# Kernel optimization log

Hardware: AMD Instinct MI355X
Metric: run time of the kernel (lower is better)

Reference implementation:

```python
import jax, jax.numpy as jnp
import numpy as np

W_DIM = 512
FREQ = 1024
CH = 512
OUT_CH = 512
SIZE = 64
SR = 64.0
BW = 2.0
MAX_BW = BW * 8.0
B = 16
K = 3


def setup_inputs() -> dict:
    key = jax.random.key(0)
    ks = jax.random.split(key, 10)
    w = jax.random.normal(ks[0], (B, W_DIM), dtype=jnp.float32)
    # SynthesisInput buffers: random unit-direction freqs scaled by uniform radius in [0, max_bw)
    f = jax.random.normal(ks[1], (FREQ, 2), dtype=jnp.float32)
    f = f / jnp.linalg.norm(f, axis=1, keepdims=True)
    freqs = f * (jax.random.uniform(ks[2], (FREQ, 1), dtype=jnp.float32) * MAX_BW)
    phases = jax.random.uniform(ks[3], (FREQ,), dtype=jnp.float32) - 0.5
    input_weight = jax.random.normal(ks[4], (CH, FREQ), dtype=jnp.float32)
    # affine: FullyConnectedLayer(w_dim, 4, weight_init=0, bias_init=[1,0,0,0])
    affine_w = jnp.zeros((4, W_DIM), dtype=jnp.float32)
    affine_b = jnp.array([1.0, 0.0, 0.0, 0.0], dtype=jnp.float32)
    # per-layer style affine (w -> in_channels), bias_init=1 (StyleGAN convention)
    style_w = jax.random.normal(ks[5], (CH, W_DIM), dtype=jnp.float32)
    style_b = jnp.ones((CH,), dtype=jnp.float32)
    conv_w = jax.random.normal(ks[6], (OUT_CH, CH, K, K), dtype=jnp.float32)
    conv_b = jnp.zeros((OUT_CH,), dtype=jnp.float32)
    return {"w": w, "affine_w": affine_w, "affine_b": affine_b, "freqs": freqs,
            "phases": phases, "input_weight": input_weight, "style_w": style_w,
            "style_b": style_b, "conv_w": conv_w, "conv_b": conv_b}


def _fc(x, weight, bias):
    # FullyConnectedLayer: weight_gain = 1/sqrt(in_features)
    gain = 1.0 / np.sqrt(weight.shape[1])
    return x @ (weight * gain).T + bias


def _synthesis_input(w, affine_w, affine_b, freqs, phases, input_weight):
    t = _fc(w, affine_w, affine_b)                                  # [B,4]
    t = t / jnp.linalg.norm(t[:, :2], axis=1, keepdims=True)
    c, s, tx, ty = t[:, 0], t[:, 1], t[:, 2], t[:, 3]
    # m = m_r @ m_t (only the 2x3 top block matters)
    rot = jnp.stack([jnp.stack([c, -s], -1), jnp.stack([s, c], -1)], 1)  # [B,2,2]
    trans = jnp.stack([-tx, -ty], -1)                               # [B,2]
    shift = jnp.einsum('bij,bj->bi', rot, trans)                    # [B,2]
    phases_b = phases[None, :] + jnp.einsum('fi,bi->bf', freqs, shift)
    freqs_b = jnp.einsum('fi,bij->bfj', freqs, rot)                 # [B,F,2]
    amp = jnp.clip(1.0 - (jnp.linalg.norm(freqs_b, axis=2) - BW) / (SR / 2.0 - BW), 0.0, 1.0)
    # affine_grid(theta=diag(0.5*size/sr)=0.5, align_corners=False)
    theta00 = 0.5 * SIZE / SR
    xs = ((jnp.arange(SIZE, dtype=jnp.float32) + 0.5) / SIZE * 2.0 - 1.0) * theta00
    ys = ((jnp.arange(SIZE, dtype=jnp.float32) + 0.5) / SIZE * 2.0 - 1.0) * theta00
    gx, gy = jnp.meshgrid(xs, ys)                                   # [H,W]
    grid = jnp.stack([gx, gy], axis=-1)                             # [H,W,2]
    x = jnp.einsum('hwi,bfi->bhwf', grid, freqs_b) + phases_b[:, None, None, :]
    x = jnp.sin(x * (2.0 * np.pi)) * amp[:, None, None, :]
    effect_freq = jnp.sum((jnp.linalg.norm(freqs, axis=-1) < BW).astype(jnp.float32))
    x = jnp.einsum('bhwf,cf->bchw', x, input_weight / jnp.sqrt(effect_freq))
    return x                                                        # [B,CH,H,W]


def _modulated_conv2d(x, weight, s, padding=1):
    # demodulate: pre-normalize w and s
    w_hat = weight * jax.lax.rsqrt(jnp.mean(jnp.square(weight), axis=(1, 2, 3), keepdims=True))
    s_hat = s * jax.lax.rsqrt(jnp.mean(jnp.square(s)))
    # dcoefs[b,o] = rsqrt(sum_ikl (w[o,i,k,l]*s[b,i])^2 + eps)
    dcoefs = jax.lax.rsqrt(jnp.einsum('oikl,bi->bo', jnp.square(w_hat), jnp.square(s_hat)) + 1e-8)
    # grouped-per-sample conv == scale input channels by s, conv with base w, scale out by dcoefs
    x = x * s_hat[:, :, None, None]
    y = jax.lax.conv_general_dilated(x, w_hat, window_strides=(1, 1),
                                     padding=[(padding, padding), (padding, padding)],
                                     dimension_numbers=('NCHW', 'OIHW', 'NCHW'))
    return y * dcoefs[:, :, None, None]


def reference(w, affine_w, affine_b, freqs, phases, input_weight, style_w, style_b, conv_w, conv_b):
    x = _synthesis_input(w, affine_w, affine_b, freqs, phases, input_weight)
    s = _fc(w, style_w, style_b)                                    # [B,CH]
    y = _modulated_conv2d(x, conv_w, s, padding=K // 2)
    y = y + conv_b[None, :, None, None]
    y = jnp.where(y >= 0, y, 0.2 * y) * np.sqrt(2.0)                # lrelu + gain (bias_act)
    y = jnp.clip(y, -256.0, 256.0)                                  # conv_clamp
    return y
```

## Files before the change

kernel.cpp:

```cpp
#include <hip/hip_runtime.h>

typedef __attribute__((ext_vector_type(4))) float f32x4;
typedef __attribute__((ext_vector_type(8))) __bf16 bf16x8;

__device__ __forceinline__ unsigned short f2bf(float f) {
  unsigned int u = __builtin_bit_cast(unsigned int, f);
  return (unsigned short)((u + 0x7FFFu + ((u >> 16) & 1u)) >> 16);
}

__device__ __forceinline__ float sin2pi(float x) {
#if __has_builtin(__builtin_amdgcn_sinf) && __has_builtin(__builtin_amdgcn_fractf)
  return __builtin_amdgcn_sinf(__builtin_amdgcn_fractf(x));
#else
  return __sinf(x * 6.283185307179586f);
#endif
}

__device__ __forceinline__ void gll16(const void* g, void* l) {
  __builtin_amdgcn_global_load_lds(
      (const __attribute__((address_space(1))) void*)g,
      (__attribute__((address_space(3))) void*)l, 16, 0, 0);
}

template <int W>
__device__ __forceinline__ void vmwait() {
  if constexpr (W == 0) asm volatile("s_waitcnt vmcnt(0)" ::: "memory");
  else if constexpr (W == 2) asm volatile("s_waitcnt vmcnt(2)" ::: "memory");
  else if constexpr (W == 4) asm volatile("s_waitcnt vmcnt(4)" ::: "memory");
  else if constexpr (W == 6) asm volatile("s_waitcnt vmcnt(6)" ::: "memory");
  else if constexpr (W == 8) asm volatile("s_waitcnt vmcnt(8)" ::: "memory");
}

#define CFENCE() asm volatile("" ::: "memory")

__global__ void prep_freq_k(const float* __restrict__ w, const float* __restrict__ affine_w,
                            const float* __restrict__ affine_b, const float* __restrict__ freqs,
                            const float* __restrict__ phases, float4* __restrict__ freq_data,
                            float* __restrict__ scal) {
  const int b = blockIdx.x, tid = threadIdx.x;
  const int wv = tid >> 6, lane = tid & 63;
  __shared__ float tdot[4];
  __shared__ float par[4];
  __shared__ float scnt;
  float sum = 0.f;
  for (int i = lane; i < 512; i += 64) sum += w[b * 512 + i] * affine_w[wv * 512 + i];
#pragma unroll
  for (int o = 32; o > 0; o >>= 1) sum += __shfl_down(sum, o);
  if (lane == 0) tdot[wv] = sum;
  if (tid == 0) scnt = 0.f;
  __syncthreads();
  if (tid == 0) {
    const float gain = 0.04419417382415922f;
    float t0 = tdot[0] * gain + affine_b[0];
    float t1 = tdot[1] * gain + affine_b[1];
    float t2 = tdot[2] * gain + affine_b[2];
    float t3 = tdot[3] * gain + affine_b[3];
    float inv = 1.f / sqrtf(t0 * t0 + t1 * t1);
    float c = t0 * inv, s = t1 * inv, tx = t2 * inv, ty = t3 * inv;
    par[0] = c; par[1] = s;
    par[2] = -c * tx + s * ty;
    par[3] = -s * tx - c * ty;
  }
  __syncthreads();
  const float c = par[0], s = par[1], sh0 = par[2], sh1 = par[3];
  float cnt = 0.f;
  for (int f = tid; f < 1024; f += 256) {
    float fx = freqs[2 * f], fy = freqs[2 * f + 1];
    float fb0 = fx * c + fy * s;
    float fb1 = fy * c - fx * s;
    float ph = phases[f] + fx * sh0 + fy * sh1;
    float nb = sqrtf(fb0 * fb0 + fb1 * fb1);
    float amp = fminf(fmaxf(1.f - (nb - 2.f) * (1.f / 30.f), 0.f), 1.f);
    float4 v; v.x = fb0; v.y = fb1; v.z = ph; v.w = amp;
    freq_data[(b << 10) + f] = v;
    if (sqrtf(fx * fx + fy * fy) < 2.f) cnt += 1.f;
  }
  if (b == 0) {
    atomicAdd(&scnt, cnt);
    __syncthreads();
    if (tid == 0) scal[0] = 1.f / sqrtf(scnt);
  }
}

__global__ void style_k(const float* __restrict__ w, const float* __restrict__ style_w,
                        const float* __restrict__ style_b, float* __restrict__ s_out) {
  int gt = blockIdx.x * 256 + threadIdx.x;
  int idx = gt >> 2, part = gt & 3;
  int b = idx >> 9, c = idx & 511;
  const float4* wr = (const float4*)(w + b * 512) + part * 32;
  const float4* sr = (const float4*)(style_w + (size_t)c * 512) + part * 32;
  float sum = 0.f;
#pragma unroll 4
  for (int i = 0; i < 32; ++i) {
    float4 a = wr[i], q = sr[i];
    sum += a.x * q.x + a.y * q.y + a.z * q.z + a.w * q.w;
  }
  sum += __shfl_xor(sum, 1);
  sum += __shfl_xor(sum, 2);
  if (part == 0) s_out[idx] = sum * 0.04419417382415922f + style_b[c];
}

__global__ void convw_prep_k(const float* __restrict__ conv_w, float* __restrict__ wsumT,
                             unsigned short* __restrict__ bt_conv) {
  const int o = blockIdx.x, tid = threadIdx.x;
  __shared__ float red[256];
  float sum = 0.f;
  for (int i = tid; i < 4608; i += 256) { float v = conv_w[o * 4608 + i]; sum += v * v; }
  red[tid] = sum;
  __syncthreads();
  for (int off = 128; off > 0; off >>= 1) {
    if (tid < off) red[tid] += red[tid + off];
    __syncthreads();
  }
  const float rn = rsqrtf(red[0] * (1.f / 4608.f));
  for (int i = tid; i < 512; i += 256) {
    float sq = 0.f;
#pragma unroll
    for (int kl = 0; kl < 9; ++kl) {
      float v = conv_w[(o * 512 + i) * 9 + kl];
      sq += v * v;
      bt_conv[o * 4608 + kl * 512 + i] = f2bf(v * rn);
    }
    wsumT[i * 512 + o] = sq * rn * rn;
  }
}

__global__ void iw_cast_k(const float* __restrict__ iw, unsigned short* __restrict__ iw_bf) {
  int i = blockIdx.x * 256 + threadIdx.x;
  iw_bf[i] = f2bf(iw[i]);
}

__global__ void shat_dcoef_k(const float* __restrict__ s, const float* __restrict__ wsumT,
                             float* __restrict__ s_hat, float* __restrict__ dcoefs) {
  const int b = blockIdx.x >> 3, og = blockIdx.x & 7, tid = threadIdx.x;
  __shared__ float red[256];
  __shared__ float sh2[512];
  __shared__ float red2[256];
  float sum = 0.f;
  for (int i = tid; i < 8192; i += 256) { float v = s[i]; sum += v * v; }
  red[tid] = sum;
  __syncthreads();
  for (int off = 128; off > 0; off >>= 1) {
    if (tid < off) red[tid] += red[tid + off];
    __syncthreads();
  }
  const float inv_rms = rsqrtf(red[0] * (1.f / 8192.f));
  for (int c = tid; c < 512; c += 256) {
    float sh = s[b * 512 + c] * inv_rms;
    if (og == 0) s_hat[b * 512 + c] = sh;
    sh2[c] = sh * sh;
  }
  __syncthreads();
  const int o = (og << 6) + (tid & 63);
  const int ic = tid >> 6;
  float acc = 0.f;
  for (int i = ic * 128; i < ic * 128 + 128; ++i) acc += wsumT[i * 512 + o] * sh2[i];
  red2[tid] = acc;
  __syncthreads();
  if (tid < 64) {
    float a = red2[tid] + red2[tid + 64] + red2[tid + 128] + red2[tid + 192];
    dcoefs[b * 512 + o] = rsqrtf(a + 1e-8f);
  }
}

__global__ void border_zero_k(unsigned short* __restrict__ xmp) {
  int idx = blockIdx.x * 256 + threadIdx.x;
  int chunk = idx & 63;
  int t = idx >> 6;
  int p = t % 260;
  int b = t / 260;
  int h, w;
  if (p < 66) { h = 0; w = p; }
  else if (p < 132) { h = 65; w = p - 66; }
  else if (p < 196) { h = p - 131; w = 0; }
  else { h = p - 195; w = 65; }
  uint4 z; z.x = 0; z.y = 0; z.z = 0; z.w = 0;
  *(uint4*)&xmp[(((size_t)b * 66 + h) * 66 + w) * 512 + chunk * 8] = z;
}

__device__ __forceinline__ void sy_sgB(char* lB, const unsigned short* iw, int n0, int d,
                                       int rb, int kt, int lane, int lsw) {
  const unsigned short* src = iw + (size_t)(n0 + rb + (lane >> 3)) * 1024 + (kt << 6) + lsw;
  gll16(src, lB + d * 32768 + rb * 128);
}

__global__ __launch_bounds__(256, 2) void synth_gemm2_k(
    const float4* __restrict__ freq_data, const unsigned short* __restrict__ iw_bf,
    const float* __restrict__ s_hat, const float* __restrict__ scal,
    unsigned short* __restrict__ xmp) {
  extern __shared__ char sl[];
  char* lA = sl;
  char* lB = sl + 16384;
  const int bid = blockIdx.x;
  const int mt = bid >> 1, nt = bid & 1;
  const int m0 = mt << 7, n0 = nt << 8;
  const int b = m0 >> 12;
  const int hbase = (m0 >> 6) & 63;
  const int tid = threadIdx.x, lane = tid & 63, wv = tid >> 6;
  const int wm = (wv >> 1) << 6, wn = (wv & 1) << 7;
  const int g = tid & 15;
  const int r0 = (tid >> 4) << 3;
  const int lsw = (((lane & 7) ^ (lane >> 3)) << 3);
  const int aswz = (((lane >> 4) << 4)) ^ ((lane & 7) << 4);
  const char* pA = lA + (size_t)(wm + (lane & 15)) * 128;
  const int browB = wn + (lane & 15);
  f32x4 acc[4][8];
#pragma unroll
  for (int mi = 0; mi < 4; ++mi)
#pragma unroll
    for (int ni = 0; ni < 8; ++ni) { f32x4 z = {0.f, 0.f, 0.f, 0.f}; acc[mi][ni] = z; }
  const float gy0 = (hbase + 0.5f) * 0.015625f - 0.5f;
  const float gy1 = (hbase + 1.5f) * 0.015625f - 0.5f;

#pragma unroll
  for (int ig = 0; ig < 8; ++ig) sy_sgB(lB, iw_bf, n0, 0, wv * 64 + ig * 8, 0, lane, lsw);
  vmwait<0>();
  __builtin_amdgcn_s_barrier();
  CFENCE();

  for (int kt = 0; kt < 16; ++kt) {
    if (kt < 15) {
#pragma unroll
      for (int ig = 0; ig < 8; ++ig)
        sy_sgB(lB, iw_bf, n0, (kt + 1) & 1, wv * 64 + ig * 8, kt + 1, lane, lsw);
    }
    const float4* fdp = freq_data + (b << 10) + (kt << 6) + (g << 2);
    float4 fd0 = fdp[0], fd1 = fdp[1], fd2 = fdp[2], fd3 = fdp[3];
#pragma unroll
    for (int j = 0; j < 8; ++j) {
      const int r = r0 + j;
      const float gx = ((r & 63) + 0.5f) * 0.015625f - 0.5f;
      const float gy = (r >> 6) ? gy1 : gy0;
      ushort4 u;
      u.x = f2bf(sin2pi(gx * fd0.x + gy * fd0.y + fd0.z) * fd0.w);
      u.y = f2bf(sin2pi(gx * fd1.x + gy * fd1.y + fd1.z) * fd1.w);
      u.z = f2bf(sin2pi(gx * fd2.x + gy * fd2.y + fd2.z) * fd2.w);
      u.w = f2bf(sin2pi(gx * fd3.x + gy * fd3.y + fd3.z) * fd3.w);
      *(ushort4*)(lA + r * 128 + ((g << 3) ^ (j << 4))) = u;
    }
    asm volatile("s_waitcnt lgkmcnt(0)" ::: "memory");
    if (kt < 15) vmwait<8>(); else vmwait<0>();
    __builtin_amdgcn_s_barrier();
    CFENCE();
    __builtin_amdgcn_sched_barrier(0);

    const char* pB = lB + ((kt & 1) << 15) + (size_t)browB * 128;
#pragma unroll
    for (int ks = 0; ks < 2; ++ks) {
      const int ao = aswz ^ (ks << 6);
      bf16x8 af[4], bq[8];
#pragma unroll
      for (int mi = 0; mi < 4; ++mi) af[mi] = *(const bf16x8*)(pA + mi * 2048 + ao);
#pragma unroll
      for (int ni = 0; ni < 8; ++ni) bq[ni] = *(const bf16x8*)(pB + ni * 2048 + ao);
      __builtin_amdgcn_s_setprio(1);
#pragma unroll
      for (int mi = 0; mi < 4; ++mi)
#pragma unroll
        for (int ni = 0; ni < 8; ++ni)
          acc[mi][ni] = __builtin_amdgcn_mfma_f32_16x16x32_bf16(af[mi], bq[ni], acc[mi][ni], 0, 0, 0);
      __builtin_amdgcn_s_setprio(0);
    }
    CFENCE();
    __builtin_amdgcn_s_barrier();
    CFENCE();
  }

  const float inv_eff = scal[0];
  const int c_lo = lane & 15, r_hi = (lane >> 4) << 2;
#pragma unroll
  for (int ni = 0; ni < 8; ++ni) {
    const int cc = n0 + wn + (ni << 4) + c_lo;
    const float sc = s_hat[b * 512 + cc] * inv_eff;
#pragma unroll
    for (int mi = 0; mi < 4; ++mi) {
#pragma unroll
      for (int j = 0; j < 4; ++j) {
        const int rr = wm + (mi << 4) + r_hi + j;
        const int hp = hbase + (rr >> 6) + 1;
        const int wp = (rr & 63) + 1;
        xmp[(((size_t)b * 66 + hp) * 66 + wp) * 512 + cc] = f2bf(acc[mi][ni][j] * sc);
      }
    }
  }
}

__device__ __forceinline__ float epi_act(float a, float dco, float cb) {
  float y = a * dco + cb;
  y = (y >= 0.f ? y : 0.2f * y) * 1.4142135623730951f;
  return fminf(fmaxf(y, -256.f), 256.f);
}

struct ConvCtx {
  const unsigned short* xmp;
  const unsigned short* bt;
  int n0, hb, b_img, lane;
  int lsw;
  int gB_rb0;
  int gA_lo;
  int gA_up;
};

__device__ __forceinline__ void tile_geom(int t, int& dh, int& dw, int& kc, int& koff) {
  const int kc8 = t / 9;
  const int off = t - 9 * kc8;
  dh = off / 3;
  dw = off - 3 * dh;
  kc = kc8 << 6;
  koff = off * 512 + kc;
}

__device__ __forceinline__ void sgA(char* lds, const ConvCtx& c, int d, int rb,
                                    int dh, int dw, int kc) {
  const int r = rb + (c.lane >> 3);
  const int h = c.hb + (r >> 6) + dh;
  const int w = (r & 63) + dw;
  const unsigned short* src = c.xmp + (((size_t)c.b_img * 66 + h) * 66 + w) * 512 + kc + c.lsw;
  gll16(src, lds + d * 32768 + rb * 128);
}

__device__ __forceinline__ void sgB(char* lds, const ConvCtx& c, int d, int rb, int koff) {
  const int row = c.n0 + rb + (c.lane >> 3);
  const unsigned short* src = c.bt + (size_t)row * 4608 + koff + c.lsw;
  gll16(src, lds + 65536 + d * 32768 + rb * 128);
}

template <bool STG>
__device__ __forceinline__ void conv_tile1(char* lds, const ConvCtx& c, f32x4 (&acc)[8][4],
                                           const char* pA, const char* pB, int aswz0, int t) {
  int dh1, dw1, kc1, koff1;
  tile_geom(t + 1, dh1, dw1, kc1, koff1);
  const int D = t & 1, Dn = D ^ 1;
  const int db = D << 15;
  const int a0 = aswz0, a1 = aswz0 ^ 64;

  vmwait<0>();
  __builtin_amdgcn_s_barrier();
  CFENCE();
  __builtin_amdgcn_sched_barrier(0);

  bf16x8 bq[4], af[4];
#pragma unroll
  for (int ni = 0; ni < 4; ++ni) bq[ni] = *(const bf16x8*)(pB + db + ni * 2048 + a0);
#pragma unroll
  for (int i = 0; i < 4; ++i) af[i] = *(const bf16x8*)(pA + db + i * 2048 + a0);
  if (STG) {
    sgB(lds, c, Dn, c.gB_rb0, koff1);      sgB(lds, c, Dn, c.gB_rb0 + 8, koff1);
    sgB(lds, c, Dn, c.gB_rb0 + 16, koff1); sgB(lds, c, Dn, c.gB_rb0 + 24, koff1);
  }
  __builtin_amdgcn_s_setprio(1);
#pragma unroll
  for (int i = 0; i < 4; ++i)
#pragma unroll
    for (int ni = 0; ni < 4; ++ni)
      acc[i][ni] = __builtin_amdgcn_mfma_f32_16x16x32_bf16(af[i], bq[ni], acc[i][ni], 0, 0, 0);
  __builtin_amdgcn_s_setprio(0);
#pragma unroll
  for (int i = 0; i < 4; ++i) af[i] = *(const bf16x8*)(pA + db + (4 + i) * 2048 + a0);
  if (STG) {
    sgA(lds, c, Dn, c.gA_up, dh1, dw1, kc1); sgA(lds, c, Dn, c.gA_up + 8, dh1, dw1, kc1);
    sgA(lds, c, Dn, c.gA_lo, dh1, dw1, kc1); sgA(lds, c, Dn, c.gA_lo + 8, dh1, dw1, kc1);
  }
  __builtin_amdgcn_s_setprio(1);
#pragma unroll
  for (int i = 0; i < 4; ++i)
#pragma unroll
    for (int ni = 0; ni < 4; ++ni)
      acc[4 + i][ni] = __builtin_amdgcn_mfma_f32_16x16x32_bf16(af[i], bq[ni], acc[4 + i][ni], 0, 0, 0);
  __builtin_amdgcn_s_setprio(0);
#pragma unroll
  for (int ni = 0; ni < 4; ++ni) bq[ni] = *(const bf16x8*)(pB + db + ni * 2048 + a1);
#pragma unroll
  for (int i = 0; i < 4; ++i) af[i] = *(const bf16x8*)(pA + db + i * 2048 + a1);
  __builtin_amdgcn_s_setprio(1);
#pragma unroll
  for (int i = 0; i < 4; ++i)
#pragma unroll
    for (int ni = 0; ni < 4; ++ni)
      acc[i][ni] = __builtin_amdgcn_mfma_f32_16x16x32_bf16(af[i], bq[ni], acc[i][ni], 0, 0, 0);
  __builtin_amdgcn_s_setprio(0);
#pragma unroll
  for (int i = 0; i < 4; ++i) af[i] = *(const bf16x8*)(pA + db + (4 + i) * 2048 + a1);
  __builtin_amdgcn_s_setprio(1);
#pragma unroll
  for (int i = 0; i < 4; ++i)
#pragma unroll
    for (int ni = 0; ni < 4; ++ni)
      acc[4 + i][ni] = __builtin_amdgcn_mfma_f32_16x16x32_bf16(af[i], bq[ni], acc[4 + i][ni], 0, 0, 0);
  __builtin_amdgcn_s_setprio(0);
  CFENCE();
}

__global__ __launch_bounds__(512, 2) void conv_gemm8_k(
    const unsigned short* __restrict__ xmp, const unsigned short* __restrict__ bt_conv,
    const float* __restrict__ dcoefs, const float* __restrict__ conv_b,
    float* __restrict__ out) {
  extern __shared__ char lds[];
  const int tid = threadIdx.x, lane = tid & 63, wv = tid >> 6;
  const int bid = blockIdx.x;
  const int wg = (bid & 7) * 64 + (bid >> 3);
  const int mt = wg >> 1, nt = wg & 1;
  const int m0 = mt << 8, n0 = nt << 8;
  const int b_img = m0 >> 12;
  const int hb = (m0 >> 6) & 63;
  const int wm = (wv >> 2) << 7, wn = (wv & 3) << 6;

  ConvCtx c;
  c.xmp = xmp; c.bt = bt_conv;
  c.n0 = n0; c.hb = hb; c.b_img = b_img; c.lane = lane;
  c.lsw = (((lane & 7) ^ (lane >> 3)) << 3);
  c.gB_rb0 = (((wv & 3) >> 1) << 7) + (((wv & 1) | ((wv >> 2) << 1)) << 5);
  c.gA_lo = wm + ((wv & 3) << 4);
  c.gA_up = c.gA_lo + 64;

  const char* pA = lds + (size_t)(wm + (lane & 15)) * 128;
  const char* pB = lds + 65536 + (size_t)(wn + (lane & 15)) * 128;
  const int aswz0 = (((lane >> 4) << 4)) ^ ((lane & 7) << 4);

  f32x4 acc[8][4];
#pragma unroll
  for (int mi = 0; mi < 8; ++mi)
#pragma unroll
    for (int ni = 0; ni < 4; ++ni) { f32x4 z = {0.f, 0.f, 0.f, 0.f}; acc[mi][ni] = z; }

  sgB(lds, c, 0, c.gB_rb0, 0);       sgB(lds, c, 0, c.gB_rb0 + 8, 0);
  sgB(lds, c, 0, c.gB_rb0 + 16, 0);  sgB(lds, c, 0, c.gB_rb0 + 24, 0);
  sgA(lds, c, 0, c.gA_up, 0, 0, 0);  sgA(lds, c, 0, c.gA_up + 8, 0, 0, 0);
  sgA(lds, c, 0, c.gA_lo, 0, 0, 0);  sgA(lds, c, 0, c.gA_lo + 8, 0, 0, 0);

  for (int t = 0; t < 71; ++t) conv_tile1<true>(lds, c, acc, pA, pB, aswz0, t);
  conv_tile1<false>(lds, c, acc, pA, pB, aswz0, 71);

  const int c_lo = lane & 15, r_hi = (lane >> 4) << 2;
#pragma unroll
  for (int ni = 0; ni < 4; ++ni) {
    const int oo = n0 + wn + (ni << 4) + c_lo;
    const float dco = dcoefs[b_img * 512 + oo];
    const float cb = conv_b[oo];
#pragma unroll
    for (int mi = 0; mi < 8; ++mi) {
      const int rr = wm + (mi << 4) + r_hi;
      const int hh = hb + (rr >> 6);
      const int w0 = rr & 63;
      float4 v;
      v.x = epi_act(acc[mi][ni][0], dco, cb);
      v.y = epi_act(acc[mi][ni][1], dco, cb);
      v.z = epi_act(acc[mi][ni][2], dco, cb);
      v.w = epi_act(acc[mi][ni][3], dco, cb);
      *(float4*)&out[(((size_t)b_img * 512 + oo) * 64 + hh) * 64 + w0] = v;
    }
  }
}

extern "C" void kernel_launch(void* const* d_in, const int* in_sizes, int n_in,
                              void* d_out, int out_size, void* d_ws, size_t ws_size,
                              hipStream_t stream) {
  (void)in_sizes; (void)n_in; (void)out_size;
  const float* w        = (const float*)d_in[0];
  const float* affine_w = (const float*)d_in[1];
  const float* affine_b = (const float*)d_in[2];
  const float* freqs    = (const float*)d_in[3];
  const float* phases   = (const float*)d_in[4];
  const float* input_weight = (const float*)d_in[5];
  const float* style_w  = (const float*)d_in[6];
  const float* style_b  = (const float*)d_in[7];
  const float* conv_w   = (const float*)d_in[8];
  const float* conv_b   = (const float*)d_in[9];
  float* out = (float*)d_out;

  char* p = (char*)d_ws;
  float4* freq_data = (float4*)p;               p += (size_t)16 * 1024 * 16;
  float* scal = (float*)p;                      p += 256;
  float* s_buf = (float*)p;                     p += 8192 * 4;
  float* s_hat = (float*)p;                     p += 8192 * 4;
  float* wsumT = (float*)p;                     p += (size_t)512 * 512 * 4;
  float* dcoefs = (float*)p;                    p += 8192 * 4;
  unsigned short* iw_bf = (unsigned short*)p;   p += (size_t)512 * 1024 * 2;
  unsigned short* bt_conv = (unsigned short*)p; p += (size_t)512 * 4608 * 2;
  unsigned short* xmp = (unsigned short*)p;     p += (size_t)16 * 66 * 66 * 512 * 2;
  if (ws_size < (size_t)(p - (char*)d_ws)) return;

  (void)hipFuncSetAttribute((const void*)conv_gemm8_k,
                            hipFuncAttributeMaxDynamicSharedMemorySize, 131072);
  (void)hipFuncSetAttribute((const void*)synth_gemm2_k,
                            hipFuncAttributeMaxDynamicSharedMemorySize, 81920);

  border_zero_k<<<1040, 256, 0, stream>>>(xmp);
  prep_freq_k<<<16, 256, 0, stream>>>(w, affine_w, affine_b, freqs, phases, freq_data, scal);
  style_k<<<128, 256, 0, stream>>>(w, style_w, style_b, s_buf);
  convw_prep_k<<<512, 256, 0, stream>>>(conv_w, wsumT, bt_conv);
  iw_cast_k<<<2048, 256, 0, stream>>>(input_weight, iw_bf);
  shat_dcoef_k<<<128, 256, 0, stream>>>(s_buf, wsumT, s_hat, dcoefs);
  synth_gemm2_k<<<1024, 256, 81920, stream>>>(freq_data, iw_bf, s_hat, scal, xmp);
  conv_gemm8_k<<<512, 512, 131072, stream>>>(xmp, bt_conv, dcoefs, conv_b, out);
}
```

Before: 411.9 us.

## Widen synthesis GEMM tile to full N so Fourier features are computed once

The synthesis GEMM now uses 512-thread blocks that cover all 512 output channels per 128-row M tile, instead of splitting N across two blocks. Each sine feature is therefore generated once rather than twice, and the B tile held in LDS doubles to 64KB per stage. Block indices are also swizzled across XCDs. In exchange, LDS use grows to 144KB, which likely allows only one block per CU despite the launch bound of 2.

```diff
diff --git a/kernel.cpp b/kernel.cpp
--- a/kernel.cpp
+++ b/kernel.cpp
@@ -178,13 +178,13 @@
   *(uint4*)&xmp[(((size_t)b * 66 + h) * 66 + w) * 512 + chunk * 8] = z;
 }
 
-__device__ __forceinline__ void sy_sgB(char* lB, const unsigned short* iw, int n0, int d,
+__device__ __forceinline__ void sy_sgB(char* lB, const unsigned short* iw, int d,
                                        int rb, int kt, int lane, int lsw) {
-  const unsigned short* src = iw + (size_t)(n0 + rb + (lane >> 3)) * 1024 + (kt << 6) + lsw;
-  gll16(src, lB + d * 32768 + rb * 128);
-}
-
-__global__ __launch_bounds__(256, 2) void synth_gemm2_k(
+  const unsigned short* src = iw + (size_t)(rb + (lane >> 3)) * 1024 + (kt << 6) + lsw;
+  gll16(src, lB + d * 65536 + rb * 128);
+}
+
+__global__ __launch_bounds__(512, 2) void synth_gemm4_k(
     const float4* __restrict__ freq_data, const unsigned short* __restrict__ iw_bf,
     const float* __restrict__ s_hat, const float* __restrict__ scal,
     unsigned short* __restrict__ xmp) {
@@ -192,14 +192,15 @@
   char* lA = sl;
   char* lB = sl + 16384;
   const int bid = blockIdx.x;
-  const int mt = bid >> 1, nt = bid & 1;
-  const int m0 = mt << 7, n0 = nt << 8;
+  const int wg = (bid & 7) * 64 + (bid >> 3);
+  const int m0 = wg << 7;
   const int b = m0 >> 12;
   const int hbase = (m0 >> 6) & 63;
   const int tid = threadIdx.x, lane = tid & 63, wv = tid >> 6;
-  const int wm = (wv >> 1) << 6, wn = (wv & 1) << 7;
-  const int g = tid & 15;
-  const int r0 = (tid >> 4) << 3;
+  const int wm = (wv >> 2) << 6;
+  const int wn = (wv & 3) << 7;
+  const int g = tid & 31;
+  const int r0 = (tid >> 5) << 3;
   const int lsw = (((lane & 7) ^ (lane >> 3)) << 3);
   const int aswz = (((lane >> 4) << 4)) ^ ((lane & 7) << 4);
   const char* pA = lA + (size_t)(wm + (lane & 15)) * 128;
@@ -213,7 +214,7 @@
   const float gy1 = (hbase + 1.5f) * 0.015625f - 0.5f;
 
 #pragma unroll
-  for (int ig = 0; ig < 8; ++ig) sy_sgB(lB, iw_bf, n0, 0, wv * 64 + ig * 8, 0, lane, lsw);
+  for (int ig = 0; ig < 8; ++ig) sy_sgB(lB, iw_bf, 0, wv * 64 + ig * 8, 0, lane, lsw);
   vmwait<0>();
   __builtin_amdgcn_s_barrier();
   CFENCE();
@@ -222,21 +223,19 @@
     if (kt < 15) {
 #pragma unroll
       for (int ig = 0; ig < 8; ++ig)
-        sy_sgB(lB, iw_bf, n0, (kt + 1) & 1, wv * 64 + ig * 8, kt + 1, lane, lsw);
-    }
-    const float4* fdp = freq_data + (b << 10) + (kt << 6) + (g << 2);
-    float4 fd0 = fdp[0], fd1 = fdp[1], fd2 = fdp[2], fd3 = fdp[3];
+        sy_sgB(lB, iw_bf, (kt + 1) & 1, wv * 64 + ig * 8, kt + 1, lane, lsw);
+    }
+    const float4* fdp = freq_data + (b << 10) + (kt << 6) + (g << 1);
+    float4 fd0 = fdp[0], fd1 = fdp[1];
 #pragma unroll
     for (int j = 0; j < 8; ++j) {
       const int r = r0 + j;
       const float gx = ((r & 63) + 0.5f) * 0.015625f - 0.5f;
       const float gy = (r >> 6) ? gy1 : gy0;
-      ushort4 u;
+      ushort2 u;
       u.x = f2bf(sin2pi(gx * fd0.x + gy * fd0.y + fd0.z) * fd0.w);
       u.y = f2bf(sin2pi(gx * fd1.x + gy * fd1.y + fd1.z) * fd1.w);
-      u.z = f2bf(sin2pi(gx * fd2.x + gy * fd2.y + fd2.z) * fd2.w);
-      u.w = f2bf(sin2pi(gx * fd3.x + gy * fd3.y + fd3.z) * fd3.w);
-      *(ushort4*)(lA + r * 128 + ((g << 3) ^ (j << 4))) = u;
+      *(ushort2*)(lA + r * 128 + ((g << 2) ^ ((r & 7) << 4))) = u;
     }
     asm volatile("s_waitcnt lgkmcnt(0)" ::: "memory");
     if (kt < 15) vmwait<8>(); else vmwait<0>();
@@ -244,7 +243,7 @@
     CFENCE();
     __builtin_amdgcn_sched_barrier(0);
 
-    const char* pB = lB + ((kt & 1) << 15) + (size_t)browB * 128;
+    const char* pB = lB + ((kt & 1) << 16) + (size_t)browB * 128;
 #pragma unroll
     for (int ks = 0; ks < 2; ++ks) {
       const int ao = aswz ^ (ks << 6);
@@ -270,7 +269,7 @@
   const int c_lo = lane & 15, r_hi = (lane >> 4) << 2;
 #pragma unroll
   for (int ni = 0; ni < 8; ++ni) {
-    const int cc = n0 + wn + (ni << 4) + c_lo;
+    const int cc = wn + (ni << 4) + c_lo;
     const float sc = s_hat[b * 512 + cc] * inv_eff;
 #pragma unroll
     for (int mi = 0; mi < 4; ++mi) {
@@ -482,8 +481,8 @@
 
   (void)hipFuncSetAttribute((const void*)conv_gemm8_k,
                             hipFuncAttributeMaxDynamicSharedMemorySize, 131072);
-  (void)hipFuncSetAttribute((const void*)synth_gemm2_k,
-                            hipFuncAttributeMaxDynamicSharedMemorySize, 81920);
+  (void)hipFuncSetAttribute((const void*)synth_gemm4_k,
+                            hipFuncAttributeMaxDynamicSharedMemorySize, 147456);
 
   border_zero_k<<<1040, 256, 0, stream>>>(xmp);
   prep_freq_k<<<16, 256, 0, stream>>>(w, affine_w, affine_b, freqs, phases, freq_data, scal);
@@ -491,6 +490,6 @@
   convw_prep_k<<<512, 256, 0, stream>>>(conv_w, wsumT, bt_conv);
   iw_cast_k<<<2048, 256, 0, stream>>>(input_weight, iw_bf);
   shat_dcoef_k<<<128, 256, 0, stream>>>(s_buf, wsumT, s_hat, dcoefs);
-  synth_gemm2_k<<<1024, 256, 81920, stream>>>(freq_data, iw_bf, s_hat, scal, xmp);
+  synth_gemm4_k<<<512, 512, 147456, stream>>>(freq_data, iw_bf, s_hat, scal, xmp);
   conv_gemm8_k<<<512, 512, 131072, stream>>>(xmp, bt_conv, dcoefs, conv_b, out);
 }
```

Result: no change. 414.1 us (+0.5%).
